# Kernel tuning notes

Hardware: AMD Instinct MI355X
Metric: run time of the kernel (lower is better)

Reference implementation:

```python
import jax, jax.numpy as jnp
import numpy as np

D = 1024        # hidden_size = input_size = output_size
E = 8           # num_experts
K = 2           # top-k
TEMP = 1.0      # router temperature


def setup_inputs() -> dict:
    key = jax.random.key(0)
    ks = jax.random.split(key, 7)
    s = 0.02
    x = jax.random.normal(ks[0], (4, 2048, D), dtype=jnp.float32)
    w_router = jax.random.normal(ks[1], (D, E), dtype=jnp.float32) * s
    w1 = jax.random.normal(ks[2], (E, D, D), dtype=jnp.float32) * s
    b1 = jnp.zeros((E, D), dtype=jnp.float32)
    w2 = jax.random.normal(ks[3], (E, D, D), dtype=jnp.float32) * s
    b2 = jnp.zeros((E, D), dtype=jnp.float32)
    return {"x": x, "w_router": w_router, "w1": w1, "b1": b1, "w2": w2, "b2": b2}


def reference(x, w_router, w1, b1, w2, b2):
    B, S, _ = x.shape
    # Router: temperature-scaled logits, softmax, top-k
    logits = jnp.einsum('bsd,de->bse', x, w_router) / TEMP          # [B,S,E]
    probs = jax.nn.softmax(logits, axis=-1)
    top_k_probs, top_k_idx = jax.lax.top_k(probs, K)                # [B,S,K]
    xt = x.reshape(-1, D)                                           # [T,D]
    idx = top_k_idx.reshape(-1, K)                                  # [T,K]
    pk = top_k_probs.reshape(-1, K)                                 # [T,K]
    # Dense expert eval: every expert on every token (faithful to source)
    h = jax.nn.gelu(jnp.einsum('td,edh->eth', xt, w1) + b1[:, None, :])
    expert_out = jnp.einsum('eth,ehd->etd', h, w2) + b2[:, None, :]  # [E,T,D]
    expert_out = jnp.transpose(expert_out, (1, 0, 2))                # [T,E,D]
    # Gather selected experts and combine with routing probs
    sel = jnp.take_along_axis(expert_out, idx[:, :, None], axis=1)   # [T,K,D]
    combined = jnp.sum(sel * pk[:, :, None], axis=1)                 # [T,D]
    return combined.reshape(B, S, D), logits
```

## Files before the change

### kernel.cpp

```cpp
#include <hip/hip_runtime.h>
#include <hip/hip_bf16.h>

#define DH 1024
#define NE 8
#define NT 8192
#define NTK 16384
#define BM 128
#define BN 256
#define NSUB 32

typedef __bf16 bf16x8 __attribute__((ext_vector_type(8)));
typedef float f32x4 __attribute__((ext_vector_type(4)));
typedef unsigned short u16;
typedef u16 u16x8 __attribute__((ext_vector_type(8)));
typedef u16 u16x4 __attribute__((ext_vector_type(4)));

__device__ __forceinline__ u16 f2bf(float f) {
  union { float f; unsigned u; } v; v.f = f;
  return (u16)((v.u + 0x7fffu + ((v.u >> 16) & 1u)) >> 16);
}
__device__ __forceinline__ float bf2f(u16 h) {
  union { unsigned u; float f; } v; v.u = ((unsigned)h) << 16;
  return v.f;
}
__device__ __forceinline__ float gelu_tanh(float v) {
  float y = 0.7978845608028654f * (v + 0.044715f * v * v * v);
  float t = 1.f - 2.f / (1.f + __expf(2.f * y));
  return 0.5f * v * (1.f + t);
}

__device__ __forceinline__ void gload_lds16(const u16* g, u16* l) {
  __builtin_amdgcn_global_load_lds(
      (const __attribute__((address_space(1))) void*)g,
      (__attribute__((address_space(3))) void*)l, 16, 0, 0);
}

__global__ __launch_bounds__(256) void prep_transpose(
    const float* __restrict__ w1, const float* __restrict__ w2,
    u16* __restrict__ w1t, u16* __restrict__ w2t) {
  __shared__ float tile[64][65];
  int z = blockIdx.z;
  const float* src = (z < NE) ? (w1 + (size_t)z * DH * DH) : (w2 + (size_t)(z - NE) * DH * DH);
  u16* dst = (z < NE) ? (w1t + (size_t)z * DH * DH) : (w2t + (size_t)(z - NE) * DH * DH);
  int d0 = blockIdx.y * 64, n0 = blockIdx.x * 64;
  int tid = threadIdx.x;
  int r16 = tid >> 4;
  int c4 = (tid & 15) * 4;
#pragma unroll
  for (int it = 0; it < 4; ++it) {
    int rr = it * 16 + r16;
    float4 v = *(const float4*)&src[(size_t)(d0 + rr) * DH + n0 + c4];
    tile[rr][c4] = v.x; tile[rr][c4 + 1] = v.y;
    tile[rr][c4 + 2] = v.z; tile[rr][c4 + 3] = v.w;
  }
  __syncthreads();
#pragma unroll
  for (int it = 0; it < 4; ++it) {
    int n = it * 16 + r16;
    u16x4 o;
    o[0] = f2bf(tile[c4][n]);     o[1] = f2bf(tile[c4 + 1][n]);
    o[2] = f2bf(tile[c4 + 2][n]); o[3] = f2bf(tile[c4 + 3][n]);
    *(u16x4*)&dst[(size_t)(n0 + n) * DH + d0 + c4] = o;
  }
}

__global__ __launch_bounds__(256) void router_kernel(
    const float* __restrict__ x, const float* __restrict__ wr,
    float* __restrict__ logits_out, int* __restrict__ tkidx,
    float* __restrict__ tkp, int* __restrict__ counts,
    u16* __restrict__ xb) {
  __shared__ float wsh[NE][DH + 8];
  __shared__ int hist[NE];
  int tid = threadIdx.x;
  for (int i = tid; i < DH * NE; i += 256) {
    int d = i >> 3, e = i & 7;
    wsh[e][d] = wr[i];
  }
  if (tid < NE) hist[tid] = 0;
  __syncthreads();

  int lane = tid & 63;
  int wv = tid >> 6;
  int t0 = blockIdx.x * 32 + wv * 8;
#pragma unroll 1
  for (int i = 0; i < 8; ++i) {
    int t = t0 + i;
    const float4* xp = (const float4*)(x + (size_t)t * DH);
    u16* xbrow = xb + (size_t)t * DH;
    float a[8] = {0.f, 0.f, 0.f, 0.f, 0.f, 0.f, 0.f, 0.f};
#pragma unroll
    for (int it = 0; it < 4; ++it) {
      float4 xv = xp[it * 64 + lane];
      int d0 = (it * 64 + lane) * 4;
      u16x4 c4;
      c4[0] = f2bf(xv.x); c4[1] = f2bf(xv.y); c4[2] = f2bf(xv.z); c4[3] = f2bf(xv.w);
      *(u16x4*)(xbrow + d0) = c4;
#pragma unroll
      for (int e = 0; e < 8; ++e) {
        float4 w4 = *(const float4*)&wsh[e][d0];
        a[e] += xv.x * w4.x + xv.y * w4.y + xv.z * w4.z + xv.w * w4.w;
      }
    }
#pragma unroll
    for (int off = 32; off; off >>= 1) {
#pragma unroll
      for (int e = 0; e < 8; ++e) a[e] += __shfl_xor(a[e], off, 64);
    }
    if (lane < 8) logits_out[(size_t)t * NE + lane] = a[lane];
    if (lane == 0) {
      float m1 = a[0]; int i1 = 0;
#pragma unroll
      for (int e = 1; e < 8; ++e) if (a[e] > m1) { m1 = a[e]; i1 = e; }
      float m2 = -3.4e38f; int i2 = 0;
#pragma unroll
      for (int e = 0; e < 8; ++e) if (e != i1 && a[e] > m2) { m2 = a[e]; i2 = e; }
      float den = 0.f;
#pragma unroll
      for (int e = 0; e < 8; ++e) den += expf(a[e] - m1);
      tkidx[2 * t] = i1; tkidx[2 * t + 1] = i2;
      tkp[2 * t] = 1.0f / den;
      tkp[2 * t + 1] = expf(m2 - m1) / den;
      atomicAdd(&hist[i1], 1);
      atomicAdd(&hist[i2], 1);
    }
  }
  __syncthreads();
  if (tid < NE) atomicAdd(&counts[tid], hist[tid]);
}

__global__ void offsets_kernel(const int* __restrict__ counts,
                               int* __restrict__ offs, int* __restrict__ cur) {
  if (threadIdx.x == 0) {
    int s = 0;
    for (int e = 0; e < NE; ++e) { offs[e] = s; s += counts[e]; cur[e] = 0; }
    offs[NE] = s;
  }
}

__global__ __launch_bounds__(1024) void scatter_kernel(
    const int* __restrict__ tkidx, const float* __restrict__ tkp,
    const int* __restrict__ offs, int* __restrict__ cur,
    int* __restrict__ rows, int* __restrict__ posof, float* __restrict__ pp) {
  __shared__ int h[NE];
  __shared__ int base[NE];
  int tid = threadIdx.x;
  int gid = blockIdx.x * 1024 + tid;
  if (tid < NE) h[tid] = 0;
  __syncthreads();
  int e = tkidx[gid];
  int myrank = atomicAdd(&h[e], 1);
  __syncthreads();
  if (tid < NE) base[tid] = atomicAdd(&cur[tid], h[tid]);
  __syncthreads();
  int pos = offs[e] + base[e] + myrank;
  rows[pos] = gid >> 1;
  posof[gid] = pos;
  pp[pos] = tkp[gid];
}

template <int GELU>
__global__ __launch_bounds__(512, 4) void gemm_kernel(
    const u16* __restrict__ A, const u16* __restrict__ W,
    const float* __restrict__ bias, const int* __restrict__ counts,
    const int* __restrict__ offs, const int* __restrict__ rows,
    u16* __restrict__ outb) {
  int e = blockIdx.x;
  int q = blockIdx.y;
  int cnt = counts[e];
  int nm = (cnt + BM - 1) / BM;
  if (q >= nm * 4) return;
  int m0 = (q >> 2) * BM;
  int n0 = (q & 3) * BN;
  int seg = offs[e];

  __shared__ __attribute__((aligned(16))) u16 lds[3][12288];

  int tid = threadIdx.x;
  int lane = tid & 63;
  int wv = tid >> 6;

  int srow = tid >> 2;
  int sc8 = ((tid & 3) ^ ((srow >> 1) & 3)) * 8;
  int gi = m0 + srow;
  int cl = gi < cnt ? gi : cnt - 1;
  int arow = GELU ? rows[seg + cl] : (seg + cl);
  const u16* aSrc = A + (size_t)arow * DH + sc8;
  const u16* bSrc0 = W + (size_t)e * DH * DH + (size_t)(n0 + srow) * DH + sc8;
  const u16* bSrc1 = bSrc0 + (size_t)128 * DH;

  int wb = wv * 512;
  auto stage = [&](int slot, int s) {
    int k0 = s * 32;
    u16* base = &lds[slot][0];
    gload_lds16(aSrc + k0, base + wb);
    gload_lds16(bSrc0 + k0, base + 4096 + wb);
    gload_lds16(bSrc1 + k0, base + 8192 + wb);
  };

  int lr = lane & 15;
  int quad = lane >> 4;
  int chunkOff = (quad ^ ((lr >> 1) & 3)) * 8;
  int wm = wv >> 2, wn = wv & 3;
  int wrr = wm * 64, wcc = wn * 64;

  int aOff[4], bOff[4];
#pragma unroll
  for (int m = 0; m < 4; ++m) aOff[m] = (wrr + m * 16 + lr) * 32 + chunkOff;
#pragma unroll
  for (int n = 0; n < 4; ++n) bOff[n] = 4096 + (wcc + n * 16 + lr) * 32 + chunkOff;

  f32x4 acc[4][4] = {};

  auto computeSub = [&](const u16* S) {
    bf16x8 af[4], bf[4];
#pragma unroll
    for (int m = 0; m < 4; ++m) af[m] = *(const bf16x8*)(S + aOff[m]);
#pragma unroll
    for (int n = 0; n < 4; ++n) bf[n] = *(const bf16x8*)(S + bOff[n]);
    __builtin_amdgcn_s_setprio(1);
#pragma unroll
    for (int m = 0; m < 4; ++m)
#pragma unroll
      for (int n = 0; n < 4; ++n)
        acc[m][n] = __builtin_amdgcn_mfma_f32_16x16x32_bf16(af[m], bf[n], acc[m][n], 0, 0, 0);
    __builtin_amdgcn_s_setprio(0);
  };

  stage(0, 0);
  stage(1, 1);
#pragma unroll 1
  for (int s = 0; s < NSUB - 2; ++s) {
    stage((s + 2) % 3, s + 2);
    asm volatile("s_waitcnt vmcnt(6)" ::: "memory");
    __builtin_amdgcn_s_barrier();
    computeSub(&lds[s % 3][0]);
    __builtin_amdgcn_s_barrier();
  }
  asm volatile("s_waitcnt vmcnt(3)" ::: "memory");
  __builtin_amdgcn_s_barrier();
  computeSub(&lds[(NSUB - 2) % 3][0]);
  __builtin_amdgcn_s_barrier();
  asm volatile("s_waitcnt vmcnt(0)" ::: "memory");
  __builtin_amdgcn_s_barrier();
  computeSub(&lds[(NSUB - 1) % 3][0]);

  int r4 = quad * 4;
  const float* be = bias + (size_t)e * DH;
#pragma unroll
  for (int m = 0; m < 4; ++m) {
#pragma unroll
    for (int n = 0; n < 4; ++n) {
      int col = n0 + wcc + n * 16 + lr;
      float bvv = be[col];
#pragma unroll
      for (int j = 0; j < 4; ++j) {
        int gr = m0 + wrr + m * 16 + r4 + j;
        if (gr < cnt) {
          float v = acc[m][n][j] + bvv;
          if (GELU) v = gelu_tanh(v);
          outb[(size_t)(seg + gr) * DH + col] = f2bf(v);
        }
      }
    }
  }
}

__global__ __launch_bounds__(256) void combine_kernel(
    const u16* __restrict__ eo, const float* __restrict__ tkp,
    const int* __restrict__ posof, float* __restrict__ out) {
  int gid = blockIdx.x * 256 + threadIdx.x;
  int t = gid >> 8;
  int n = (gid & 255) * 4;
  float p0 = tkp[2 * t], p1 = tkp[2 * t + 1];
  int q0 = posof[2 * t], q1 = posof[2 * t + 1];
  u16x4 a = *(const u16x4*)(eo + (size_t)q0 * DH + n);
  u16x4 b = *(const u16x4*)(eo + (size_t)q1 * DH + n);
  float4 o;
  o.x = p0 * bf2f(a[0]) + p1 * bf2f(b[0]);
  o.y = p0 * bf2f(a[1]) + p1 * bf2f(b[1]);
  o.z = p0 * bf2f(a[2]) + p1 * bf2f(b[2]);
  o.w = p0 * bf2f(a[3]) + p1 * bf2f(b[3]);
  *(float4*)(out + (size_t)t * DH + n) = o;
}

extern "C" void kernel_launch(void* const* d_in, const int* in_sizes, int n_in,
                              void* d_out, int out_size, void* d_ws, size_t ws_size,
                              hipStream_t stream) {
  const float* x = (const float*)d_in[0];
  const float* w_router = (const float*)d_in[1];
  const float* w1 = (const float*)d_in[2];
  const float* b1 = (const float*)d_in[3];
  const float* w2 = (const float*)d_in[4];
  const float* b2 = (const float*)d_in[5];
  float* out = (float*)d_out;
  float* logits = out + (size_t)NT * DH;

  char* ws = (char*)d_ws;
  size_t off = 0;
  auto alloc = [&](size_t bytes) -> void* {
    void* p = ws + off;
    off = (off + bytes + 255) & ~(size_t)255;
    return p;
  };
  int* ctrl = (int*)alloc(256);
  int* counts = ctrl;
  int* cur = ctrl + 8;
  int* offs = ctrl + 16;
  int* tkidx = (int*)alloc((size_t)NTK * 4);
  float* tkp = (float*)alloc((size_t)NTK * 4);
  int* rows = (int*)alloc((size_t)NTK * 4);
  int* posof = (int*)alloc((size_t)NTK * 4);
  float* pp = (float*)alloc((size_t)NTK * 4);
  u16* w1t = (u16*)alloc((size_t)NE * DH * DH * 2);
  u16* w2t = (u16*)alloc((size_t)NE * DH * DH * 2);
  u16* hbuf = (u16*)alloc((size_t)NTK * DH * 2);
  u16* eo = (u16*)alloc((size_t)NTK * DH * 2);
  u16* xb = eo;

  hipMemsetAsync(ctrl, 0, 256, stream);

  prep_transpose<<<dim3(16, 16, 16), 256, 0, stream>>>(w1, w2, w1t, w2t);
  router_kernel<<<NT / 32, 256, 0, stream>>>(x, w_router, logits, tkidx, tkp, counts, xb);
  offsets_kernel<<<1, 64, 0, stream>>>(counts, offs, cur);
  scatter_kernel<<<NTK / 1024, 1024, 0, stream>>>(tkidx, tkp, offs, cur, rows, posof, pp);
  gemm_kernel<1><<<dim3(8, 544, 1), 512, 0, stream>>>(xb, w1t, b1, counts, offs, rows, hbuf);
  gemm_kernel<0><<<dim3(8, 544, 1), 512, 0, stream>>>(hbuf, w2t, b2, counts, offs, rows, eo);
  combine_kernel<<<NT, 256, 0, stream>>>(eo, tkp, posof, out);
}
```

Before: 182.0 us.

## Merge weight transpose with router, fold offsets into consumers, widen combine loads

The weight transpose/bf16 conversion and the router are combined into one launch, selected by block index, and share a single LDS buffer. The offsets kernel is removed: scatter and the GEMMs now compute prefix sums from counts themselves. The combine kernel moves to 8-element loads per thread with half the blocks. Together these cut two kernel launches and let the transpose and router blocks overlap, at the cost of every block reserving the larger shared-memory footprint, which can lower occupancy for the transpose blocks.

```diff
diff --git a/kernel.cpp b/kernel.cpp
--- a/kernel.cpp
+++ b/kernel.cpp
@@ -35,43 +35,50 @@
       (__attribute__((address_space(3))) void*)l, 16, 0, 0);
 }
 
-__global__ __launch_bounds__(256) void prep_transpose(
+__global__ __launch_bounds__(256) void prep_kernel(
     const float* __restrict__ w1, const float* __restrict__ w2,
-    u16* __restrict__ w1t, u16* __restrict__ w2t) {
-  __shared__ float tile[64][65];
-  int z = blockIdx.z;
-  const float* src = (z < NE) ? (w1 + (size_t)z * DH * DH) : (w2 + (size_t)(z - NE) * DH * DH);
-  u16* dst = (z < NE) ? (w1t + (size_t)z * DH * DH) : (w2t + (size_t)(z - NE) * DH * DH);
-  int d0 = blockIdx.y * 64, n0 = blockIdx.x * 64;
-  int tid = threadIdx.x;
-  int r16 = tid >> 4;
-  int c4 = (tid & 15) * 4;
-#pragma unroll
-  for (int it = 0; it < 4; ++it) {
-    int rr = it * 16 + r16;
-    float4 v = *(const float4*)&src[(size_t)(d0 + rr) * DH + n0 + c4];
-    tile[rr][c4] = v.x; tile[rr][c4 + 1] = v.y;
-    tile[rr][c4 + 2] = v.z; tile[rr][c4 + 3] = v.w;
-  }
-  __syncthreads();
-#pragma unroll
-  for (int it = 0; it < 4; ++it) {
-    int n = it * 16 + r16;
-    u16x4 o;
-    o[0] = f2bf(tile[c4][n]);     o[1] = f2bf(tile[c4 + 1][n]);
-    o[2] = f2bf(tile[c4 + 2][n]); o[3] = f2bf(tile[c4 + 3][n]);
-    *(u16x4*)&dst[(size_t)(n0 + n) * DH + d0 + c4] = o;
-  }
-}
-
-__global__ __launch_bounds__(256) void router_kernel(
     const float* __restrict__ x, const float* __restrict__ wr,
+    u16* __restrict__ w1t, u16* __restrict__ w2t,
     float* __restrict__ logits_out, int* __restrict__ tkidx,
     float* __restrict__ tkp, int* __restrict__ counts,
     u16* __restrict__ xb) {
-  __shared__ float wsh[NE][DH + 8];
-  __shared__ int hist[NE];
+  __shared__ __attribute__((aligned(16))) char smem[33088];
+  int bid = blockIdx.x;
   int tid = threadIdx.x;
+
+  if (bid < 4096) {
+    float (*tile)[65] = (float(*)[65])smem;
+    int z = bid >> 8;
+    int rem = bid & 255;
+    const float* src = (z < NE) ? (w1 + (size_t)z * DH * DH)
+                                : (w2 + (size_t)(z - NE) * DH * DH);
+    u16* dst = (z < NE) ? (w1t + (size_t)z * DH * DH)
+                        : (w2t + (size_t)(z - NE) * DH * DH);
+    int d0 = (rem >> 4) * 64, n0 = (rem & 15) * 64;
+    int r16 = tid >> 4;
+    int c4 = (tid & 15) * 4;
+#pragma unroll
+    for (int it = 0; it < 4; ++it) {
+      int rr = it * 16 + r16;
+      float4 v = *(const float4*)&src[(size_t)(d0 + rr) * DH + n0 + c4];
+      tile[rr][c4] = v.x; tile[rr][c4 + 1] = v.y;
+      tile[rr][c4 + 2] = v.z; tile[rr][c4 + 3] = v.w;
+    }
+    __syncthreads();
+#pragma unroll
+    for (int it = 0; it < 4; ++it) {
+      int n = it * 16 + r16;
+      u16x4 o;
+      o[0] = f2bf(tile[c4][n]);     o[1] = f2bf(tile[c4 + 1][n]);
+      o[2] = f2bf(tile[c4 + 2][n]); o[3] = f2bf(tile[c4 + 3][n]);
+      *(u16x4*)&dst[(size_t)(n0 + n) * DH + d0 + c4] = o;
+    }
+    return;
+  }
+
+  float (*wsh)[DH + 8] = (float(*)[DH + 8])smem;
+  int* hist = (int*)(smem + NE * (DH + 8) * sizeof(float));
+  int rb = bid - 4096;
   for (int i = tid; i < DH * NE; i += 256) {
     int d = i >> 3, e = i & 7;
     wsh[e][d] = wr[i];
@@ -81,7 +88,7 @@
 
   int lane = tid & 63;
   int wv = tid >> 6;
-  int t0 = blockIdx.x * 32 + wv * 8;
+  int t0 = rb * 32 + wv * 8;
 #pragma unroll 1
   for (int i = 0; i < 8; ++i) {
     int t = t0 + i;
@@ -128,31 +135,27 @@
   if (tid < NE) atomicAdd(&counts[tid], hist[tid]);
 }
 
-__global__ void offsets_kernel(const int* __restrict__ counts,
-                               int* __restrict__ offs, int* __restrict__ cur) {
-  if (threadIdx.x == 0) {
-    int s = 0;
-    for (int e = 0; e < NE; ++e) { offs[e] = s; s += counts[e]; cur[e] = 0; }
-    offs[NE] = s;
-  }
-}
-
 __global__ __launch_bounds__(1024) void scatter_kernel(
     const int* __restrict__ tkidx, const float* __restrict__ tkp,
-    const int* __restrict__ offs, int* __restrict__ cur,
+    const int* __restrict__ counts, int* __restrict__ cur,
     int* __restrict__ rows, int* __restrict__ posof, float* __restrict__ pp) {
   __shared__ int h[NE];
   __shared__ int base[NE];
+  __shared__ int offsL[NE];
   int tid = threadIdx.x;
   int gid = blockIdx.x * 1024 + tid;
   if (tid < NE) h[tid] = 0;
+  if (tid == 0) {
+    int s = 0;
+    for (int e = 0; e < NE; ++e) { offsL[e] = s; s += counts[e]; }
+  }
   __syncthreads();
   int e = tkidx[gid];
   int myrank = atomicAdd(&h[e], 1);
   __syncthreads();
   if (tid < NE) base[tid] = atomicAdd(&cur[tid], h[tid]);
   __syncthreads();
-  int pos = offs[e] + base[e] + myrank;
+  int pos = offsL[e] + base[e] + myrank;
   rows[pos] = gid >> 1;
   posof[gid] = pos;
   pp[pos] = tkp[gid];
@@ -162,8 +165,7 @@
 __global__ __launch_bounds__(512, 4) void gemm_kernel(
     const u16* __restrict__ A, const u16* __restrict__ W,
     const float* __restrict__ bias, const int* __restrict__ counts,
-    const int* __restrict__ offs, const int* __restrict__ rows,
-    u16* __restrict__ outb) {
+    const int* __restrict__ rows, u16* __restrict__ outb) {
   int e = blockIdx.x;
   int q = blockIdx.y;
   int cnt = counts[e];
@@ -171,7 +173,8 @@
   if (q >= nm * 4) return;
   int m0 = (q >> 2) * BM;
   int n0 = (q & 3) * BN;
-  int seg = offs[e];
+  int seg = 0;
+  for (int i = 0; i < e; ++i) seg += counts[i];
 
   __shared__ __attribute__((aligned(16))) u16 lds[3][12288];
 
@@ -269,18 +272,23 @@
     const u16* __restrict__ eo, const float* __restrict__ tkp,
     const int* __restrict__ posof, float* __restrict__ out) {
   int gid = blockIdx.x * 256 + threadIdx.x;
-  int t = gid >> 8;
-  int n = (gid & 255) * 4;
+  int t = gid >> 7;
+  int n = (gid & 127) * 8;
   float p0 = tkp[2 * t], p1 = tkp[2 * t + 1];
   int q0 = posof[2 * t], q1 = posof[2 * t + 1];
-  u16x4 a = *(const u16x4*)(eo + (size_t)q0 * DH + n);
-  u16x4 b = *(const u16x4*)(eo + (size_t)q1 * DH + n);
-  float4 o;
-  o.x = p0 * bf2f(a[0]) + p1 * bf2f(b[0]);
-  o.y = p0 * bf2f(a[1]) + p1 * bf2f(b[1]);
-  o.z = p0 * bf2f(a[2]) + p1 * bf2f(b[2]);
-  o.w = p0 * bf2f(a[3]) + p1 * bf2f(b[3]);
-  *(float4*)(out + (size_t)t * DH + n) = o;
+  u16x8 a = *(const u16x8*)(eo + (size_t)q0 * DH + n);
+  u16x8 b = *(const u16x8*)(eo + (size_t)q1 * DH + n);
+  float4 o0, o1;
+  o0.x = p0 * bf2f(a[0]) + p1 * bf2f(b[0]);
+  o0.y = p0 * bf2f(a[1]) + p1 * bf2f(b[1]);
+  o0.z = p0 * bf2f(a[2]) + p1 * bf2f(b[2]);
+  o0.w = p0 * bf2f(a[3]) + p1 * bf2f(b[3]);
+  o1.x = p0 * bf2f(a[4]) + p1 * bf2f(b[4]);
+  o1.y = p0 * bf2f(a[5]) + p1 * bf2f(b[5]);
+  o1.z = p0 * bf2f(a[6]) + p1 * bf2f(b[6]);
+  o1.w = p0 * bf2f(a[7]) + p1 * bf2f(b[7]);
+  *(float4*)(out + (size_t)t * DH + n) = o0;
+  *(float4*)(out + (size_t)t * DH + n + 4) = o1;
 }
 
 extern "C" void kernel_launch(void* const* d_in, const int* in_sizes, int n_in,
@@ -305,7 +313,6 @@
   int* ctrl = (int*)alloc(256);
   int* counts = ctrl;
   int* cur = ctrl + 8;
-  int* offs = ctrl + 16;
   int* tkidx = (int*)alloc((size_t)NTK * 4);
   float* tkp = (float*)alloc((size_t)NTK * 4);
   int* rows = (int*)alloc((size_t)NTK * 4);
@@ -319,11 +326,11 @@
 
   hipMemsetAsync(ctrl, 0, 256, stream);
 
-  prep_transpose<<<dim3(16, 16, 16), 256, 0, stream>>>(w1, w2, w1t, w2t);
-  router_kernel<<<NT / 32, 256, 0, stream>>>(x, w_router, logits, tkidx, tkp, counts, xb);
-  offsets_kernel<<<1, 64, 0, stream>>>(counts, offs, cur);
-  scatter_kernel<<<NTK / 1024, 1024, 0, stream>>>(tkidx, tkp, offs, cur, rows, posof, pp);
-  gemm_kernel<1><<<dim3(8, 544, 1), 512, 0, stream>>>(xb, w1t, b1, counts, offs, rows, hbuf);
-  gemm_kernel<0><<<dim3(8, 544, 1), 512, 0, stream>>>(hbuf, w2t, b2, counts, offs, rows, eo);
-  combine_kernel<<<NT, 256, 0, stream>>>(eo, tkp, posof, out);
-}
+  prep_kernel<<<4352, 256, 0, stream>>>(w1, w2, x, w_router, w1t, w2t,
+                                        logits, tkidx, tkp, counts, xb);
+  scatter_kernel<<<NTK / 1024, 1024, 0, stream>>>(tkidx, tkp, counts, cur,
+                                                  rows, posof, pp);
+  gemm_kernel<1><<<dim3(8, 544, 1), 512, 0, stream>>>(xb, w1t, b1, counts, rows, hbuf);
+  gemm_kernel<0><<<dim3(8, 544, 1), 512, 0, stream>>>(hbuf, w2t, b2, counts, rows, eo);
+  combine_kernel<<<NT * DH / 8 / 256, 256, 0, stream>>>(eo, tkp, posof, out);
+}
```

Measured after the change: 187.6 us. 3.1% more time.
